# Optimization experiments

Hardware: AMD Instinct MI355X
Metric: run time of the kernel (lower is better)

The kernel has to match this reference:

```python
import jax, jax.numpy as jnp
import numpy as np

SEQ_LEN, BATCH, HID, ATT = 2048, 64, 512, 512


def setup_inputs() -> dict:
    key = jax.random.key(0)
    k1, k2, k3, k4, k5, k6 = jax.random.split(key, 6)
    return {
        "dec_out": jax.random.normal(k1, (BATCH, HID), dtype=jnp.float32),
        "enc_outs": jax.random.normal(k2, (SEQ_LEN, BATCH, HID), dtype=jnp.float32),
        "W_s": jax.random.normal(k3, (ATT, HID), dtype=jnp.float32) * (1.0 / np.sqrt(HID)),
        "W_t": jax.random.normal(k4, (ATT, HID), dtype=jnp.float32) * (1.0 / np.sqrt(HID)),
        "b_t": jax.random.normal(k5, (ATT,), dtype=jnp.float32) * 0.01,
        "v_a": jax.random.uniform(k6, (ATT,), dtype=jnp.float32, minval=-0.05, maxval=0.05),
    }


def reference(dec_out, enc_outs, W_s, W_t, b_t, v_a):
    # enc_att: (seq_len, batch, att) = W_s @ enc_outs
    enc_att = jnp.einsum('sbh,ah->sba', enc_outs, W_s)
    # dec_att: (batch, att) = W_t @ dec_out + b_t
    dec_att = dec_out @ W_t.T + b_t
    # score(b, s) = v_a . tanh(enc_att[s,b] + dec_att[b])
    scores = jnp.einsum('sba,a->bs', jnp.tanh(enc_att + dec_att[None, :, :]), v_a)
    return scores  # (batch, seq_len)
```

## Files before the change

### kernel.cpp

```cpp
#include <hip/hip_runtime.h>

typedef __attribute__((ext_vector_type(8))) short short8;
typedef __attribute__((ext_vector_type(4))) float f32x4;

#define SEQ 2048
#define BATCH 64
#define HID 512
#define ATT 512

__device__ __forceinline__ unsigned short f2bf(float f) {
  unsigned u = __float_as_uint(f);
  u += 0x7fffu + ((u >> 16) & 1u);
  return (unsigned short)(u >> 16);
}

__device__ __forceinline__ void dma16(const void* g, void* l) {
  __builtin_amdgcn_global_load_lds(
      (const __attribute__((address_space(1))) unsigned int*)g,
      (__attribute__((address_space(3))) unsigned int*)l, 16, 0, 0);
}

__device__ __forceinline__ short8 cvt8(float4 lo, float4 hi) {
  union { unsigned u[4]; short8 s; } r;
  asm("v_cvt_pk_bf16_f32 %0, %1, %2" : "=v"(r.u[0]) : "v"(lo.x), "v"(lo.y));
  asm("v_cvt_pk_bf16_f32 %0, %1, %2" : "=v"(r.u[1]) : "v"(lo.z), "v"(lo.w));
  asm("v_cvt_pk_bf16_f32 %0, %1, %2" : "=v"(r.u[2]) : "v"(hi.x), "v"(hi.y));
  asm("v_cvt_pk_bf16_f32 %0, %1, %2" : "=v"(r.u[3]) : "v"(hi.z), "v"(hi.w));
  return r.s;
}

#define GLOADS(dst, voff, base, OFF) \
  asm volatile("global_load_dwordx4 %0, %1, %2 offset:" #OFF \
               : "=v"(dst) : "v"(voff), "s"(base))

#define BWAIT(N, b0, b1, b2, b3) \
  asm volatile("s_waitcnt vmcnt(" #N ")" \
               : "+v"(b0), "+v"(b1), "+v"(b2), "+v"(b3) :: "memory")

#define DSREAD(dst, vaddr, IMM) \
  asm volatile("ds_read_b128 %0, %1 offset:%2" \
               : "=v"(dst) : "v"(vaddr), "i"(IMM))

__global__ void bahdanau_pre(const float* __restrict__ dec_out,
                             const float* __restrict__ W_t,
                             const float* __restrict__ b_t,
                             const float* __restrict__ W_s,
                             unsigned short* __restrict__ wsb,
                             float* __restrict__ decT,
                             float* __restrict__ out) {
  ((float4*)out)[blockIdx.x * 256 + threadIdx.x] = make_float4(0.f, 0.f, 0.f, 0.f);

  if (blockIdx.x < 64) {
    const int b = blockIdx.x;
    __shared__ float drow[HID];
    for (int i = threadIdx.x; i < HID; i += 256) drow[i] = dec_out[b * HID + i];
    __syncthreads();
    for (int a = threadIdx.x; a < ATT; a += 256) {
      const float4* wr = (const float4*)(W_t + (size_t)a * HID);
      float s0 = 0.f, s1 = 0.f, s2 = 0.f, s3 = 0.f;
#pragma unroll 4
      for (int j = 0; j < HID / 4; ++j) {
        float4 w = wr[j];
        s0 = fmaf(w.x, drow[4 * j + 0], s0);
        s1 = fmaf(w.y, drow[4 * j + 1], s1);
        s2 = fmaf(w.z, drow[4 * j + 2], s2);
        s3 = fmaf(w.w, drow[4 * j + 3], s3);
      }
      decT[a * BATCH + b] = (s0 + s1) + (s2 + s3) + b_t[a];
    }
  } else {
    const int cb = blockIdx.x - 64;
    const float4* src = (const float4*)W_s;
#pragma unroll
    for (int i = 0; i < 4; ++i) {
      int idx = cb * 1024 + i * 256 + threadIdx.x;
      float4 v = src[idx];
      int a = idx >> 7;
      int h = (idx & 127) * 4;
      ushort4 o;
      o.x = f2bf(v.x); o.y = f2bf(v.y); o.z = f2bf(v.z); o.w = f2bf(v.w);
      int blk = (a >> 4) * 64 + ((h >> 3) & 3) * 16 + (a & 15);
      int dst = (h >> 5) * 16384 + blk * 8 + (h & 7);
      *(ushort4*)&wsb[dst] = o;
    }
  }
}

__global__ __launch_bounds__(256, 3)
void bahdanau_main(const float* __restrict__ enc,
                   const unsigned short* __restrict__ wsb,
                   const float* __restrict__ decT,
                   const float* __restrict__ v_a,
                   float* __restrict__ out) {
  __shared__ __align__(16) float Abuf[3][2][2048];
  __shared__ float partial[256];

  const int tid  = threadIdx.x;
  const int w    = tid >> 6;
  const int lane = tid & 63;
  const int c = lane & 15;
  const int q = lane >> 4;
  const int x7 = c & 7;
  const int bid = blockIdx.x;
  const int s = bid >> 1;
  const int h = bid & 1;
  const int n0 = h * 256 + w * 64;
  const int t0 = (s & 7) * 2;

  const char* encB = (const char*)(enc + (size_t)s * 64 * HID);

  const int am   = w * 16 + (lane >> 3);
  const int jsrc = (lane & 7) ^ (lane >> 3);
  const char* aSrc = encB + am * 2048 + jsrc * 16;

  const unsigned voff = (unsigned)(((h * 4 + w) * 256 + q * 16 + c) * 16);

  const unsigned lA = (unsigned)(size_t)(__attribute__((address_space(3))) char*)&Abuf[0][0][0];
  const unsigned loOff = lA + (unsigned)(c * 128 + (((2 * q)    ) ^ x7) * 16);
  const unsigned hiOff = lA + (unsigned)(c * 128 + (((2 * q) | 1) ^ x7) * 16);

  f32x4 acc[4][4];
#pragma unroll
  for (int nt = 0; nt < 4; ++nt)
#pragma unroll
    for (int mt = 0; mt < 4; ++mt)
      acc[mt][nt] = *(const f32x4*)(decT + (size_t)(n0 + nt * 16 + c) * 64 + mt * 16 + q * 4);

  asm volatile("s_waitcnt vmcnt(0)" ::: "memory");

  short8 bf[2][4];

#define STAGE(a, b) do { \
    const char* s_ = aSrc + (size_t)(((t0 + 2 * (a)) & 15) * 128); \
    char* d_ = (char*)&Abuf[(b)][0][0] + w * 2048; \
    dma16(s_,                d_); \
    dma16(s_ + 16384,        d_ + 1024); \
    dma16(s_ + 128,          d_ + 8192); \
    dma16(s_ + 128 + 16384,  d_ + 8192 + 1024); \
  } while (0)

#define LOADB(set, t_) do { \
    const unsigned short* bk_ = wsb + (size_t)(t_) * 16384; \
    GLOADS(bf[set][0], voff, bk_, 0); \
    GLOADS(bf[set][1], voff, bk_, 1024); \
    GLOADS(bf[set][2], voff, bk_, 2048); \
    GLOADS(bf[set][3], voff, bk_, 3072); \
  } while (0)

  STAGE(0, 0);
  STAGE(1, 1);
  LOADB(0, t0);
  asm volatile("s_waitcnt vmcnt(8)" ::: "memory");
  __builtin_amdgcn_s_barrier();

#pragma unroll
  for (int i = 0; i < 16; ++i) {
    const int g = i >> 1, j = i & 1, buf = (i >> 1) % 3;

    if (i + 1 < 16) LOADB((i + 1) & 1, (t0 + i + 1) & 15);
    if (j == 0 && g + 2 <= 7) STAGE(g + 2, (g + 2) % 3);

    if (i <= 11)      BWAIT(8, bf[i & 1][0], bf[i & 1][1], bf[i & 1][2], bf[i & 1][3]);
    else if (i <= 14) BWAIT(4, bf[i & 1][0], bf[i & 1][1], bf[i & 1][2], bf[i & 1][3]);
    else              BWAIT(0, bf[i & 1][0], bf[i & 1][1], bf[i & 1][2], bf[i & 1][3]);

    float4 lo0, hi0, lo1, hi1, lo2, hi2, lo3, hi3;
    DSREAD(lo0, loOff, (buf * 16384 + j * 8192 + 0 * 2048));
    DSREAD(hi0, hiOff, (buf * 16384 + j * 8192 + 0 * 2048));
    DSREAD(lo1, loOff, (buf * 16384 + j * 8192 + 1 * 2048));
    DSREAD(hi1, hiOff, (buf * 16384 + j * 8192 + 1 * 2048));
    DSREAD(lo2, loOff, (buf * 16384 + j * 8192 + 2 * 2048));
    DSREAD(hi2, hiOff, (buf * 16384 + j * 8192 + 2 * 2048));
    DSREAD(lo3, loOff, (buf * 16384 + j * 8192 + 3 * 2048));
    DSREAD(hi3, hiOff, (buf * 16384 + j * 8192 + 3 * 2048));
    asm volatile("s_waitcnt lgkmcnt(0)" ::: "memory");
    __builtin_amdgcn_sched_barrier(0);

    short8 af0 = cvt8(lo0, hi0);
    short8 af1 = cvt8(lo1, hi1);
    short8 af2 = cvt8(lo2, hi2);
    short8 af3 = cvt8(lo3, hi3);
#pragma unroll
    for (int nt = 0; nt < 4; ++nt) {
      acc[0][nt] = __builtin_amdgcn_mfma_f32_16x16x32_bf16(af0, bf[i & 1][nt], acc[0][nt], 0, 0, 0);
      acc[1][nt] = __builtin_amdgcn_mfma_f32_16x16x32_bf16(af1, bf[i & 1][nt], acc[1][nt], 0, 0, 0);
      acc[2][nt] = __builtin_amdgcn_mfma_f32_16x16x32_bf16(af2, bf[i & 1][nt], acc[2][nt], 0, 0, 0);
      acc[3][nt] = __builtin_amdgcn_mfma_f32_16x16x32_bf16(af3, bf[i & 1][nt], acc[3][nt], 0, 0, 0);
    }

    if (j == 1 && g < 7) __builtin_amdgcn_s_barrier();
  }
#undef STAGE
#undef LOADB

  float va[4];
#pragma unroll
  for (int nt = 0; nt < 4; ++nt) va[nt] = v_a[n0 + nt * 16 + c];

  float rowsum[4][4];
#pragma unroll
  for (int mt = 0; mt < 4; ++mt) {
#pragma unroll
    for (int r = 0; r < 4; ++r) {
      float sum = 0.f;
#pragma unroll
      for (int nt = 0; nt < 4; ++nt) {
        float x = acc[mt][nt][r];
        float e = __builtin_amdgcn_exp2f(x * 2.8853900817779268f);
        float t = 1.f - 2.f * __builtin_amdgcn_rcpf(e + 1.f);
        sum = fmaf(va[nt], t, sum);
      }
      rowsum[mt][r] = sum;
    }
  }

#pragma unroll
  for (int off = 1; off < 16; off <<= 1) {
#pragma unroll
    for (int mt = 0; mt < 4; ++mt)
#pragma unroll
      for (int r = 0; r < 4; ++r)
        rowsum[mt][r] += __shfl_xor(rowsum[mt][r], off, 64);
  }

  if (c == 0) {
#pragma unroll
    for (int mt = 0; mt < 4; ++mt)
#pragma unroll
      for (int r = 0; r < 4; ++r)
        partial[w * 64 + mt * 16 + q * 4 + r] = rowsum[mt][r];
  }
  __syncthreads();

  if (tid < 64) {
    float sum = 0.f;
#pragma unroll
    for (int ww = 0; ww < 4; ++ww) sum += partial[ww * 64 + tid];
    atomicAdd(&out[(size_t)tid * SEQ + s], sum);
  }
}

extern "C" void kernel_launch(void* const* d_in, const int* in_sizes, int n_in,
                              void* d_out, int out_size, void* d_ws, size_t ws_size,
                              hipStream_t stream) {
  const float* dec_out = (const float*)d_in[0];
  const float* enc     = (const float*)d_in[1];
  const float* W_s     = (const float*)d_in[2];
  const float* W_t     = (const float*)d_in[3];
  const float* b_t     = (const float*)d_in[4];
  const float* v_a     = (const float*)d_in[5];
  float* out = (float*)d_out;

  unsigned short* wsb = (unsigned short*)d_ws;
  float* decT = (float*)((char*)d_ws + (size_t)ATT * HID * 2);

  bahdanau_pre<<<128, 256, 0, stream>>>(dec_out, W_t, b_t, W_s, wsb, decT, out);
  bahdanau_main<<<SEQ * 2, 256, 0, stream>>>(enc, wsb, decT, v_a, out);
}
```

Measured before the change: 459.5 us.

## Stage encoder tiles via register loads with one-time bf16 conversion into LDS

Replaces direct global-to-LDS DMA of fp32 encoder tiles, where every wave reread fp32 data and converted it, with per-thread global loads into registers. Each thread converts its share to bf16 once and writes it to a double-buffered LDS tile, so LDS use is halved and each iteration reads bf16 fragments directly. It also remaps block IDs so neighbouring blocks are spread across the sequence. In exchange it adds a barrier every iteration, more register pressure for in-flight A loads, and a register-to-LDS write path with hand-tuned vmcnt waits that are fragile.

```diff
diff --git a/kernel.cpp b/kernel.cpp
--- a/kernel.cpp
+++ b/kernel.cpp
@@ -14,13 +14,7 @@
   return (unsigned short)(u >> 16);
 }
 
-__device__ __forceinline__ void dma16(const void* g, void* l) {
-  __builtin_amdgcn_global_load_lds(
-      (const __attribute__((address_space(1))) unsigned int*)g,
-      (__attribute__((address_space(3))) unsigned int*)l, 16, 0, 0);
-}
-
-__device__ __forceinline__ short8 cvt8(float4 lo, float4 hi) {
+__device__ __forceinline__ short8 cvt8(f32x4 lo, f32x4 hi) {
   union { unsigned u[4]; short8 s; } r;
   asm("v_cvt_pk_bf16_f32 %0, %1, %2" : "=v"(r.u[0]) : "v"(lo.x), "v"(lo.y));
   asm("v_cvt_pk_bf16_f32 %0, %1, %2" : "=v"(r.u[1]) : "v"(lo.z), "v"(lo.w));
@@ -36,10 +30,30 @@
 #define BWAIT(N, b0, b1, b2, b3) \
   asm volatile("s_waitcnt vmcnt(" #N ")" \
                : "+v"(b0), "+v"(b1), "+v"(b2), "+v"(b3) :: "memory")
-
-#define DSREAD(dst, vaddr, IMM) \
+#define AWAIT(N, a0, a1) \
+  asm volatile("s_waitcnt vmcnt(" #N ")" \
+               : "+v"(a0), "+v"(a1) :: "memory")
+
+#define DSREADS(dst, vaddr, IMM) \
   asm volatile("ds_read_b128 %0, %1 offset:%2" \
                : "=v"(dst) : "v"(vaddr), "i"(IMM))
+#define DSWRITE(vaddr, data, IMM) \
+  asm volatile("ds_write_b128 %0, %1 offset:%2" \
+               :: "v"(vaddr), "v"(data), "i"(IMM) : "memory")
+
+#define ALOAD(set, tt) do { \
+    unsigned va_ = voffA + (unsigned)(tt) * 128u; \
+    asm volatile("global_load_dwordx4 %0, %1, %2 offset:0"  : "=v"(aLo[set]) : "v"(va_), "s"(encB)); \
+    asm volatile("global_load_dwordx4 %0, %1, %2 offset:16" : "=v"(aHi[set]) : "v"(va_), "s"(encB)); \
+  } while (0)
+
+#define LOADB(set, t_) do { \
+    const unsigned short* bk_ = wsb + (size_t)(t_) * 16384; \
+    GLOADS(bf[set][0], voff, bk_, 0); \
+    GLOADS(bf[set][1], voff, bk_, 1024); \
+    GLOADS(bf[set][2], voff, bk_, 2048); \
+    GLOADS(bf[set][3], voff, bk_, 3072); \
+  } while (0)
 
 __global__ void bahdanau_pre(const float* __restrict__ dec_out,
                              const float* __restrict__ W_t,
@@ -92,7 +106,7 @@
                    const float* __restrict__ decT,
                    const float* __restrict__ v_a,
                    float* __restrict__ out) {
-  __shared__ __align__(16) float Abuf[3][2][2048];
+  __shared__ __align__(16) short Ab[2][2048];
   __shared__ float partial[256];
 
   const int tid  = threadIdx.x;
@@ -100,24 +114,23 @@
   const int lane = tid & 63;
   const int c = lane & 15;
   const int q = lane >> 4;
-  const int x7 = c & 7;
+
   const int bid = blockIdx.x;
-  const int s = bid >> 1;
-  const int h = bid & 1;
+  const int wid = (bid & 7) * 512 + (bid >> 3);
+  const int s = wid >> 1;
+  const int h = wid & 1;
   const int n0 = h * 256 + w * 64;
   const int t0 = (s & 7) * 2;
 
-  const char* encB = (const char*)(enc + (size_t)s * 64 * HID);
-
-  const int am   = w * 16 + (lane >> 3);
-  const int jsrc = (lane & 7) ^ (lane >> 3);
-  const char* aSrc = encB + am * 2048 + jsrc * 16;
+  const float* encB = enc + (size_t)s * 64 * HID;
+
+  const unsigned voffA = (unsigned)((w * 16 + (lane >> 2)) * 2048 + (lane & 3) * 32);
 
   const unsigned voff = (unsigned)(((h * 4 + w) * 256 + q * 16 + c) * 16);
 
-  const unsigned lA = (unsigned)(size_t)(__attribute__((address_space(3))) char*)&Abuf[0][0][0];
-  const unsigned loOff = lA + (unsigned)(c * 128 + (((2 * q)    ) ^ x7) * 16);
-  const unsigned hiOff = lA + (unsigned)(c * 128 + (((2 * q) | 1) ^ x7) * 16);
+  const unsigned lA = (unsigned)(size_t)(__attribute__((address_space(3))) char*)&Ab[0][0];
+  const unsigned rdOff = lA + (unsigned)(c * 64 + q * 16);
+  const unsigned wtOff = lA + (unsigned)((w * 16 + (lane >> 2)) * 64 + (lane & 3) * 16);
 
   f32x4 acc[4][4];
 #pragma unroll
@@ -129,57 +142,36 @@
   asm volatile("s_waitcnt vmcnt(0)" ::: "memory");
 
   short8 bf[2][4];
-
-#define STAGE(a, b) do { \
-    const char* s_ = aSrc + (size_t)(((t0 + 2 * (a)) & 15) * 128); \
-    char* d_ = (char*)&Abuf[(b)][0][0] + w * 2048; \
-    dma16(s_,                d_); \
-    dma16(s_ + 16384,        d_ + 1024); \
-    dma16(s_ + 128,          d_ + 8192); \
-    dma16(s_ + 128 + 16384,  d_ + 8192 + 1024); \
-  } while (0)
-
-#define LOADB(set, t_) do { \
-    const unsigned short* bk_ = wsb + (size_t)(t_) * 16384; \
-    GLOADS(bf[set][0], voff, bk_, 0); \
-    GLOADS(bf[set][1], voff, bk_, 1024); \
-    GLOADS(bf[set][2], voff, bk_, 2048); \
-    GLOADS(bf[set][3], voff, bk_, 3072); \
-  } while (0)
-
-  STAGE(0, 0);
-  STAGE(1, 1);
+  f32x4 aLo[2], aHi[2];
+
+  ALOAD(0, t0);
   LOADB(0, t0);
-  asm volatile("s_waitcnt vmcnt(8)" ::: "memory");
+  ALOAD(1, (t0 + 1) & 15);
+  AWAIT(6, aLo[0], aHi[0]);
+  {
+    short8 a0_ = cvt8(aLo[0], aHi[0]);
+    DSWRITE(wtOff, a0_, 0);
+  }
+  asm volatile("s_waitcnt lgkmcnt(0)" ::: "memory");
   __builtin_amdgcn_s_barrier();
 
 #pragma unroll
   for (int i = 0; i < 16; ++i) {
-    const int g = i >> 1, j = i & 1, buf = (i >> 1) % 3;
-
     if (i + 1 < 16) LOADB((i + 1) & 1, (t0 + i + 1) & 15);
-    if (j == 0 && g + 2 <= 7) STAGE(g + 2, (g + 2) % 3);
-
-    if (i <= 11)      BWAIT(8, bf[i & 1][0], bf[i & 1][1], bf[i & 1][2], bf[i & 1][3]);
-    else if (i <= 14) BWAIT(4, bf[i & 1][0], bf[i & 1][1], bf[i & 1][2], bf[i & 1][3]);
-    else              BWAIT(0, bf[i & 1][0], bf[i & 1][1], bf[i & 1][2], bf[i & 1][3]);
-
-    float4 lo0, hi0, lo1, hi1, lo2, hi2, lo3, hi3;
-    DSREAD(lo0, loOff, (buf * 16384 + j * 8192 + 0 * 2048));
-    DSREAD(hi0, hiOff, (buf * 16384 + j * 8192 + 0 * 2048));
-    DSREAD(lo1, loOff, (buf * 16384 + j * 8192 + 1 * 2048));
-    DSREAD(hi1, hiOff, (buf * 16384 + j * 8192 + 1 * 2048));
-    DSREAD(lo2, loOff, (buf * 16384 + j * 8192 + 2 * 2048));
-    DSREAD(hi2, hiOff, (buf * 16384 + j * 8192 + 2 * 2048));
-    DSREAD(lo3, loOff, (buf * 16384 + j * 8192 + 3 * 2048));
-    DSREAD(hi3, hiOff, (buf * 16384 + j * 8192 + 3 * 2048));
+    if (i + 2 < 16) ALOAD((i + 2) & 1, (t0 + i + 2) & 15);
+
+    short8 af0, af1, af2, af3;
+    DSREADS(af0, rdOff, ((i & 1) * 4096 + 0 * 1024));
+    DSREADS(af1, rdOff, ((i & 1) * 4096 + 1 * 1024));
+    DSREADS(af2, rdOff, ((i & 1) * 4096 + 2 * 1024));
+    DSREADS(af3, rdOff, ((i & 1) * 4096 + 3 * 1024));
     asm volatile("s_waitcnt lgkmcnt(0)" ::: "memory");
     __builtin_amdgcn_sched_barrier(0);
 
-    short8 af0 = cvt8(lo0, hi0);
-    short8 af1 = cvt8(lo1, hi1);
-    short8 af2 = cvt8(lo2, hi2);
-    short8 af3 = cvt8(lo3, hi3);
+    if (i <= 13)      BWAIT(8, bf[i & 1][0], bf[i & 1][1], bf[i & 1][2], bf[i & 1][3]);
+    else if (i == 14) BWAIT(6, bf[i & 1][0], bf[i & 1][1], bf[i & 1][2], bf[i & 1][3]);
+    else              BWAIT(0, bf[i & 1][0], bf[i & 1][1], bf[i & 1][2], bf[i & 1][3]);
+
 #pragma unroll
     for (int nt = 0; nt < 4; ++nt) {
       acc[0][nt] = __builtin_amdgcn_mfma_f32_16x16x32_bf16(af0, bf[i & 1][nt], acc[0][nt], 0, 0, 0);
@@ -188,10 +180,15 @@
       acc[3][nt] = __builtin_amdgcn_mfma_f32_16x16x32_bf16(af3, bf[i & 1][nt], acc[3][nt], 0, 0, 0);
     }
 
-    if (j == 1 && g < 7) __builtin_amdgcn_s_barrier();
-  }
-#undef STAGE
-#undef LOADB
+    if (i + 1 < 16) {
+      if (i <= 13) AWAIT(6, aLo[(i + 1) & 1], aHi[(i + 1) & 1]);
+      else         AWAIT(4, aLo[(i + 1) & 1], aHi[(i + 1) & 1]);
+      short8 an_ = cvt8(aLo[(i + 1) & 1], aHi[(i + 1) & 1]);
+      DSWRITE(wtOff, an_, (((i + 1) & 1) * 4096));
+      asm volatile("s_waitcnt lgkmcnt(0)" ::: "memory");
+      __builtin_amdgcn_s_barrier();
+    }
+  }
 
   float va[4];
 #pragma unroll
```

New measurement: 471.9 us. 1.03x slower.
